# Performance work log

Measured on AMD Instinct MI355X. Metric: run time of the kernel, lower is better.

Reference implementation:

```python
import jax, jax.numpy as jnp
import numpy as np

LN_EPS = 1e-5  # torch nn.LayerNorm default
ATT_EPS = 1e-8  # episilon added to sqrt(dk)

B, S, D = 16, 2048, 1024


def setup_inputs() -> dict:
    key = jax.random.key(0)
    ks = jax.random.split(key, 5)
    Q = jax.random.normal(ks[0], (B, S, D), dtype=jnp.float32)
    K = jax.random.normal(ks[1], (B, S, D), dtype=jnp.float32)
    V = jax.random.normal(ks[2], (B, S, D), dtype=jnp.float32)
    # xavier_normal for square DxD: std = sqrt(2/(D+D)) = 1/sqrt(D)
    std = 1.0 / np.sqrt(D)
    W1 = jax.random.normal(ks[3], (D, D), dtype=jnp.float32) * std
    W2 = jax.random.normal(ks[4], (D, D), dtype=jnp.float32) * std
    b1 = jnp.zeros((D,), dtype=jnp.float32)
    b2 = jnp.zeros((D,), dtype=jnp.float32)
    ln_gamma = jnp.ones((D,), dtype=jnp.float32)
    ln_beta = jnp.zeros((D,), dtype=jnp.float32)
    return {"Q": Q, "K": K, "V": V, "W1": W1, "b1": b1, "W2": W2, "b2": b2,
            "ln_gamma": ln_gamma, "ln_beta": ln_beta}


def _layer_norm(x, gamma, beta):
    mu = jnp.mean(x, axis=-1, keepdims=True)
    var = jnp.mean(jnp.square(x - mu), axis=-1, keepdims=True)
    return (x - mu) * jax.lax.rsqrt(var + LN_EPS) * gamma + beta


def reference(Q, K, V, W1, b1, W2, b2, ln_gamma, ln_beta):
    d = Q.shape[-1]
    scale = 1.0 / (jnp.sqrt(jnp.float32(max(1.0, d))) + ATT_EPS)
    # scores: (B, Sq, Sk)
    scores = jnp.einsum('bqd,bkd->bqk', Q, K) * scale
    attn = jax.nn.softmax(scores, axis=-1)
    V_att = jnp.einsum('bqk,bkd->bqd', attn, V)
    X = _layer_norm(Q + V_att, ln_gamma, ln_beta)
    ffn = jnp.einsum('bqd,ed->bqe', jax.nn.relu(jnp.einsum('bqd,hd->bqh', X, W1) + b1), W2) + b2
    return _layer_norm(ffn + X, ln_gamma, ln_beta)
```

## Files before the change

### kernel.cpp

```cpp
#include <hip/hip_runtime.h>
#include <cmath>
#include <cstdint>

#define LN_EPS 1e-5f

typedef __bf16 bf16x8 __attribute__((ext_vector_type(8)));
typedef float f32x4 __attribute__((ext_vector_type(4)));
typedef unsigned short u16x8 __attribute__((ext_vector_type(8)));
typedef unsigned short u16x4 __attribute__((ext_vector_type(4)));

__device__ inline float b2f(unsigned short u) {
    union { unsigned int ui; float f; } x; x.ui = ((unsigned int)u) << 16; return x.f;
}
__device__ inline unsigned short f2b(float f) {
    union { float f; unsigned int ui; } x; x.f = f;
    unsigned int u = x.ui;
    return (unsigned short)((u + 0x7FFFu + ((u >> 16) & 1u)) >> 16);
}

__global__ void cvt_kernel(const float* __restrict__ in, unsigned short* __restrict__ out,
                           long n, float scale) {
    long i = ((long)blockIdx.x * blockDim.x + threadIdx.x) * 8;
    long stride = (long)gridDim.x * blockDim.x * 8;
    for (; i < n; i += stride) {
        float4 a = *reinterpret_cast<const float4*>(in + i);
        float4 b = *reinterpret_cast<const float4*>(in + i + 4);
        u16x8 o;
        o[0] = f2b(a.x * scale); o[1] = f2b(a.y * scale); o[2] = f2b(a.z * scale); o[3] = f2b(a.w * scale);
        o[4] = f2b(b.x * scale); o[5] = f2b(b.y * scale); o[6] = f2b(b.z * scale); o[7] = f2b(b.w * scale);
        *reinterpret_cast<u16x8*>(out + i) = o;
    }
}

__global__ void transpose_kernel(const float* __restrict__ V, unsigned short* __restrict__ Vt,
                                 int S, int D) {
    __shared__ float t[32][33];
    int b = blockIdx.z;
    int s0 = blockIdx.x * 32, d0 = blockIdx.y * 32;
    int tx = threadIdx.x & 31, ty = threadIdx.x >> 5;
    const float* Vb = V + (long)b * S * D;
    unsigned short* Vtb = Vt + (long)b * S * D;
#pragma unroll
    for (int r = 0; r < 4; ++r)
        t[ty + r * 8][tx] = Vb[(long)(s0 + ty + r * 8) * D + d0 + tx];
    __syncthreads();
#pragma unroll
    for (int r = 0; r < 4; ++r)
        Vtb[(long)(d0 + ty + r * 8) * S + s0 + tx] = f2b(t[tx][ty + r * 8]);
}

#define GBK 64

__device__ inline void gload16(const unsigned short* g, unsigned short* l) {
    __builtin_amdgcn_global_load_lds((const __attribute__((address_space(1))) void*)g,
                                     (__attribute__((address_space(3))) void*)l, 16, 0, 0);
}

__device__ inline void stage_half(const unsigned short* gRowBase, int ldk, int k0,
                                  unsigned short* ldsHalf, int tid) {
#pragma unroll
    for (int l = 0; l < 2; ++l) {
        int g = l * 512 + tid;
        int row = g >> 3;
        int lg = (g & 7) ^ (row & 7);
        gload16(gRowBase + (long)row * ldk + k0 + lg * 8, ldsHalf + g * 8);
    }
}

__device__ inline bf16x8 frag_ld(const unsigned short* ldsHalf, int rowInHalf, int kgran) {
    int sw = kgran ^ (rowInHalf & 7);
    return *reinterpret_cast<const bf16x8*>(ldsHalf + rowInHalf * 64 + sw * 8);
}

#define GMFMA(am, bn, mi, ni) \
    acc[mi][ni] = __builtin_amdgcn_mfma_f32_16x16x32_bf16(am, bn, acc[mi][ni], 0, 0, 0)

template <int MODE>
__global__ __launch_bounds__(512, 1) void gemm256(
    const unsigned short* __restrict__ A, const unsigned short* __restrict__ B,
    void* __restrict__ Cout, const float* __restrict__ aux1, const float* __restrict__ aux2,
    int N, int K, long bsA, long bsB, long bsC, float scale) {
    extern __shared__ __align__(16) unsigned short lds[];
    const int bz = blockIdx.z;
    const unsigned short* Ab = A + bz * bsA + (long)blockIdx.y * 256 * K;
    const unsigned short* Bb = B + bz * bsB + (long)blockIdx.x * 256 * K;
    const int tid = threadIdx.x;
    const int wid = tid >> 6, lane = tid & 63;
    const int wr = wid >> 2, wc = wid & 3;
    const int lr = lane & 15, kq = lane >> 4;
    const int NT = K / GBK;
    const int ccol = lane & 15, crow0 = kq * 4;
    const long m0 = (long)blockIdx.y * 256 + wr * 128;
    const long n0 = (long)blockIdx.x * 256 + wc * 64;

#define STAGE_A(tile, half) stage_half(Ab + (long)(half) * 128 * K, K, (tile) * GBK, \
        lds + (((tile) & 1) * 32768 + (half) * 8192), tid)
#define STAGE_B(tile, half) stage_half(Bb + (long)(half) * 128 * K, K, (tile) * GBK, \
        lds + (((tile) & 1) * 32768 + 16384 + (half) * 8192), tid)

    f32x4 acc[8][4];
#pragma unroll
    for (int i = 0; i < 8; ++i)
#pragma unroll
        for (int j = 0; j < 4; ++j) acc[i][j] = (f32x4){0.f, 0.f, 0.f, 0.f};
    bf16x8 a[4][2], b[4][2];

    STAGE_A(0, 0); STAGE_A(0, 1); STAGE_B(0, 0); STAGE_B(0, 1);
    STAGE_B(1, 0); STAGE_A(1, 0);
    asm volatile("s_waitcnt vmcnt(4)" ::: "memory");
    __builtin_amdgcn_s_barrier();

    for (int t = 0; t < NT; ++t) {
        const unsigned short* aB = lds + ((t & 1) * 32768 + wr * 8192);
        const unsigned short* bB = lds + ((t & 1) * 32768 + 16384 + (wc >> 1) * 8192);
        const int bRow0 = (wc & 1) * 64;
#pragma unroll
        for (int m = 0; m < 4; ++m)
#pragma unroll
            for (int ks = 0; ks < 2; ++ks)
                a[m][ks] = frag_ld(aB, m * 16 + lr, ks * 4 + kq);
#pragma unroll
        for (int n = 0; n < 2; ++n)
#pragma unroll
            for (int ks = 0; ks < 2; ++ks)
                b[n][ks] = frag_ld(bB, bRow0 + n * 16 + lr, ks * 4 + kq);
        if (t + 1 < NT) STAGE_A(t + 1, 1);
        __builtin_amdgcn_s_barrier();
        asm volatile("s_waitcnt lgkmcnt(0)" ::: "memory");
        __builtin_amdgcn_sched_barrier(0);
        __builtin_amdgcn_s_setprio(1);
#pragma unroll
        for (int m = 0; m < 4; ++m)
#pragma unroll
            for (int n = 0; n < 2; ++n)
#pragma unroll
                for (int ks = 0; ks < 2; ++ks) GMFMA(a[m][ks], b[n][ks], m, n);
        __builtin_amdgcn_s_setprio(0);
        __builtin_amdgcn_s_barrier();
#pragma unroll
        for (int n = 0; n < 2; ++n)
#pragma unroll
            for (int ks = 0; ks < 2; ++ks)
                b[2 + n][ks] = frag_ld(bB, bRow0 + (2 + n) * 16 + lr, ks * 4 + kq);
        if (t + 1 < NT) STAGE_B(t + 1, 1);
        __builtin_amdgcn_s_barrier();
        asm volatile("s_waitcnt lgkmcnt(0)" ::: "memory");
        __builtin_amdgcn_sched_barrier(0);
        __builtin_amdgcn_s_setprio(1);
#pragma unroll
        for (int m = 0; m < 4; ++m)
#pragma unroll
            for (int n = 0; n < 2; ++n)
#pragma unroll
                for (int ks = 0; ks < 2; ++ks) GMFMA(a[m][ks], b[2 + n][ks], m, 2 + n);
        __builtin_amdgcn_s_setprio(0);
        __builtin_amdgcn_s_barrier();
#pragma unroll
        for (int m = 0; m < 4; ++m)
#pragma unroll
            for (int ks = 0; ks < 2; ++ks)
                a[m][ks] = frag_ld(aB, 64 + m * 16 + lr, ks * 4 + kq);
        if (t + 2 < NT) STAGE_B(t + 2, 0);
        __builtin_amdgcn_s_barrier();
        asm volatile("s_waitcnt lgkmcnt(0)" ::: "memory");
        __builtin_amdgcn_sched_barrier(0);
        __builtin_amdgcn_s_setprio(1);
#pragma unroll
        for (int m = 0; m < 4; ++m)
#pragma unroll
            for (int n = 0; n < 2; ++n)
#pragma unroll
                for (int ks = 0; ks < 2; ++ks) GMFMA(a[m][ks], b[n][ks], 4 + m, n);
        __builtin_amdgcn_s_setprio(0);
        __builtin_amdgcn_s_barrier();
        if (t + 2 < NT) STAGE_A(t + 2, 0);
        if (t < NT - 2) asm volatile("s_waitcnt vmcnt(4)" ::: "memory");
        else            asm volatile("s_waitcnt vmcnt(0)" ::: "memory");
        __builtin_amdgcn_s_barrier();
        __builtin_amdgcn_s_setprio(1);
#pragma unroll
        for (int m = 0; m < 4; ++m)
#pragma unroll
            for (int n = 0; n < 2; ++n)
#pragma unroll
                for (int ks = 0; ks < 2; ++ks) GMFMA(a[m][ks], b[2 + n][ks], 4 + m, 2 + n);
        __builtin_amdgcn_s_setprio(0);
        __builtin_amdgcn_s_barrier();
    }

    if (MODE == 0) {
        float* sl = (float*)lds;
        unsigned short* Pout = (unsigned short*)Cout;
#pragma unroll
        for (int m = 0; m < 8; ++m) {
            float ls[4] = {0.f, 0.f, 0.f, 0.f};
#pragma unroll
            for (int n = 0; n < 4; ++n) {
                long gn = n0 + n * 16 + ccol;
#pragma unroll
                for (int r = 0; r < 4; ++r) {
                    float p = __expf(acc[m][n][r]);
                    ls[r] += p;
                    Pout[bz * bsC + (m0 + m * 16 + crow0 + r) * N + gn] = f2b(p);
                }
            }
#pragma unroll
            for (int r = 0; r < 4; ++r)
#pragma unroll
                for (int off = 8; off >= 1; off >>= 1) ls[r] += __shfl_xor(ls[r], off, 64);
            if ((lane & 15) == 0)
#pragma unroll
                for (int r = 0; r < 4; ++r)
                    sl[wc * 256 + wr * 128 + m * 16 + crow0 + r] = ls[r];
        }
        __syncthreads();
        if (wc == 0) {
#pragma unroll
            for (int rep = 0; rep < 2; ++rep) {
                int rowB = wr * 128 + rep * 64 + lane;
                float s4 = sl[0 * 256 + rowB] + sl[1 * 256 + rowB] +
                           sl[2 * 256 + rowB] + sl[3 * 256 + rowB];
                ((float*)aux1)[((long)bz * 8 + blockIdx.x) * 2048 + blockIdx.y * 256 + rowB] = s4;
            }
        }
        return;
    }

    if (MODE == 1) {
        const float* il = aux2 + (long)bz * 2048 + m0;
#pragma unroll
        for (int m = 0; m < 8; ++m)
#pragma unroll
            for (int r = 0; r < 4; ++r) {
                float cf = il[m * 16 + crow0 + r];
#pragma unroll
                for (int n = 0; n < 4; ++n) acc[m][n][r] *= cf;
            }
    }

#pragma unroll
    for (int m = 0; m < 8; ++m) {
#pragma unroll
        for (int n = 0; n < 4; ++n) {
            long gn = n0 + n * 16 + ccol;
#pragma unroll
            for (int r = 0; r < 4; ++r) {
                long gm = m0 + m * 16 + crow0 + r;
                float v = acc[m][n][r];
                if (MODE == 1) {
                    long idx = bz * bsC + gm * N + gn;
                    ((float*)Cout)[idx] = v + aux1[idx];
                } else if (MODE == 2) {
                    ((unsigned short*)Cout)[gm * N + gn] = f2b(fmaxf(v + aux1[gn], 0.f));
                } else {
                    long idx = gm * N + gn;
                    ((float*)Cout)[idx] = v + aux1[gn] + b2f(((const unsigned short*)aux2)[idx]);
                }
            }
        }
    }
#undef STAGE_A
#undef STAGE_B
}

__global__ void suminv_kernel(const float* __restrict__ stats, float* __restrict__ invL) {
    int i = blockIdx.x * 256 + threadIdx.x;
    int bz = i >> 11, row = i & 2047;
    long base = (long)bz * 8 * 2048 + row;
    float L = 0.f;
#pragma unroll
    for (int t = 0; t < 8; ++t) L += stats[base + t * 2048];
    invL[i] = 1.f / L;
}

__device__ inline float wave_sum(float v) {
#pragma unroll
    for (int off = 32; off > 0; off >>= 1) v += __shfl_xor(v, off, 64);
    return v;
}

template <bool WF32, bool WB16>
__global__ void ln_kernel(const float* __restrict__ X, const float* __restrict__ gamma,
                          const float* __restrict__ beta, float* __restrict__ outf,
                          unsigned short* __restrict__ outb) {
    __shared__ float red[8];
    long row = blockIdx.x;
    const float* x = X + row * 1024;
    int tid = threadIdx.x;
    int wv = tid >> 6, ln = tid & 63;
    float4 v = *reinterpret_cast<const float4*>(x + tid * 4);
    float s = v.x + v.y + v.z + v.w;
    float q = v.x * v.x + v.y * v.y + v.z * v.z + v.w * v.w;
    s = wave_sum(s);
    q = wave_sum(q);
    if (ln == 0) { red[wv] = s; red[4 + wv] = q; }
    __syncthreads();
    s = red[0] + red[1] + red[2] + red[3];
    q = red[4] + red[5] + red[6] + red[7];
    float mu = s * (1.f / 1024.f);
    float var = q * (1.f / 1024.f) - mu * mu;
    float rs = rsqrtf(var + LN_EPS);
    float4 g = *reinterpret_cast<const float4*>(gamma + tid * 4);
    float4 b = *reinterpret_cast<const float4*>(beta + tid * 4);
    float4 y;
    y.x = (v.x - mu) * rs * g.x + b.x;
    y.y = (v.y - mu) * rs * g.y + b.y;
    y.z = (v.z - mu) * rs * g.z + b.z;
    y.w = (v.w - mu) * rs * g.w + b.w;
    if (WF32)
        *reinterpret_cast<float4*>(outf + row * 1024 + tid * 4) = y;
    if (WB16) {
        u16x4 o;
        o[0] = f2b(y.x); o[1] = f2b(y.y); o[2] = f2b(y.z); o[3] = f2b(y.w);
        *reinterpret_cast<u16x4*>(outb + row * 1024 + tid * 4) = o;
    }
}

extern "C" void kernel_launch(void* const* d_in, const int* in_sizes, int n_in,
                              void* d_out, int out_size, void* d_ws, size_t ws_size,
                              hipStream_t stream) {
    const float* Q     = (const float*)d_in[0];
    const float* K     = (const float*)d_in[1];
    const float* V     = (const float*)d_in[2];
    const float* W1    = (const float*)d_in[3];
    const float* b1    = (const float*)d_in[4];
    const float* W2    = (const float*)d_in[5];
    const float* b2    = (const float*)d_in[6];
    const float* gamma = (const float*)d_in[7];
    const float* beta  = (const float*)d_in[8];
    float* out = (float*)d_out;

    const int Bq = 16, S = 2048, D = 1024;
    const long SD = (long)S * D;
    const long SS = (long)S * S;
    const long rows = (long)Bq * S;

    const size_t NEED = 3 * (size_t)(Bq * SD * 2) + 2 * (size_t)D * D * 2 + (size_t)(Bq * SS * 2);
    if (ws_size < NEED) return;

    char* ws = (char*)d_ws;
    unsigned short* Qb  = (unsigned short*)ws; ws += Bq * SD * 2;
    unsigned short* Kb  = (unsigned short*)ws; ws += Bq * SD * 2;
    unsigned short* Vt  = (unsigned short*)ws; ws += Bq * SD * 2;
    unsigned short* W1b = (unsigned short*)ws; ws += (long)D * D * 2;
    unsigned short* W2b = (unsigned short*)ws; ws += (long)D * D * 2;
    unsigned short* Sb  = (unsigned short*)ws; ws += Bq * SS * 2;

    unsigned short* Xb = Qb;
    unsigned short* H  = Kb;
    float*          Y  = (float*)Sb;
    float*          Xf = out;

    float* stats = (float*)W1b;
    float* invL  = stats + (long)Bq * 8 * 2048;

    (void)hipFuncSetAttribute(reinterpret_cast<const void*>(&gemm256<0>),
                              hipFuncAttributeMaxDynamicSharedMemorySize, 131072);
    (void)hipFuncSetAttribute(reinterpret_cast<const void*>(&gemm256<1>),
                              hipFuncAttributeMaxDynamicSharedMemorySize, 131072);
    (void)hipFuncSetAttribute(reinterpret_cast<const void*>(&gemm256<2>),
                              hipFuncAttributeMaxDynamicSharedMemorySize, 131072);
    (void)hipFuncSetAttribute(reinterpret_cast<const void*>(&gemm256<3>),
                              hipFuncAttributeMaxDynamicSharedMemorySize, 131072);

    const float scale = 1.0f / (sqrtf((float)D) + 1e-8f);

    cvt_kernel<<<1024, 256, 0, stream>>>(Q, Qb, Bq * SD, scale);
    cvt_kernel<<<1024, 256, 0, stream>>>(K, Kb, Bq * SD, 1.0f);
    transpose_kernel<<<dim3(S / 32, D / 32, Bq), 256, 0, stream>>>(V, Vt, S, D);

    gemm256<0><<<dim3(S / 256, S / 256, Bq), 512, 131072, stream>>>(
        Qb, Kb, Sb, stats, nullptr, S, D, SD, SD, SS, 1.0f);
    suminv_kernel<<<128, 256, 0, stream>>>(stats, invL);
    gemm256<1><<<dim3(D / 256, S / 256, Bq), 512, 131072, stream>>>(
        Sb, Vt, Xf, Q, invL, D, S, SS, SD, SD, 1.0f);

    ln_kernel<false, true><<<rows, 256, 0, stream>>>(Xf, gamma, beta, nullptr, Xb);

    cvt_kernel<<<512, 256, 0, stream>>>(W1, W1b, (long)D * D, 1.0f);
    cvt_kernel<<<512, 256, 0, stream>>>(W2, W2b, (long)D * D, 1.0f);

    gemm256<2><<<dim3(D / 256, rows / 256, 1), 512, 131072, stream>>>(
        Xb, W1b, H, b1, nullptr, D, D, 0, 0, 0, 1.0f);
    gemm256<3><<<dim3(D / 256, rows / 256, 1), 512, 131072, stream>>>(
        H, W2b, Y, b2, (const float*)Xb, D, D, 0, 0, 0, 1.0f);
    ln_kernel<true, false><<<rows, 256, 0, stream>>>(Y, gamma, beta, out, nullptr);
}
```

Baseline: 722.0 us.

## Make GEMM kernel persistent with cross-tile prefetch and restructured fragment pipeline

The GEMM kernel becomes persistent. Each block processes TPB consecutive output tiles on a 256-block grid, and the LDS double-buffer prefetch continues across tile boundaries so the next tile's loads overlap the current epilogue. The inner loop is reordered so the next k-step's A/B fragments are loaded before the last MFMA group, and the explicit lgkmcnt waits and sched barriers are removed. The attention-output epilogue now reads the residual from the scaled bf16 Q copy and rescales it, instead of reading fp32 Q, which adds some bf16 rounding error. The softmax stats scratch moves to an extra 4 KB of LDS so it does not clobber the staging buffers.

```diff
diff --git a/kernel.cpp b/kernel.cpp
--- a/kernel.cpp
+++ b/kernel.cpp
@@ -79,188 +79,235 @@
 __global__ __launch_bounds__(512, 1) void gemm256(
     const unsigned short* __restrict__ A, const unsigned short* __restrict__ B,
     void* __restrict__ Cout, const float* __restrict__ aux1, const float* __restrict__ aux2,
-    int N, int K, long bsA, long bsB, long bsC, float scale) {
+    int tX, int tY, int N, int K, long bsA, long bsB, long bsC, float scale, int TPB) {
     extern __shared__ __align__(16) unsigned short lds[];
-    const int bz = blockIdx.z;
-    const unsigned short* Ab = A + bz * bsA + (long)blockIdx.y * 256 * K;
-    const unsigned short* Bb = B + bz * bsB + (long)blockIdx.x * 256 * K;
     const int tid = threadIdx.x;
     const int wid = tid >> 6, lane = tid & 63;
     const int wr = wid >> 2, wc = wid & 3;
     const int lr = lane & 15, kq = lane >> 4;
-    const int NT = K / GBK;
+    const int NT = K >> 6;
+    const int totalKT = TPB * NT;
     const int ccol = lane & 15, crow0 = kq * 4;
-    const long m0 = (long)blockIdx.y * 256 + wr * 128;
-    const long n0 = (long)blockIdx.x * 256 + wc * 64;
-
-#define STAGE_A(tile, half) stage_half(Ab + (long)(half) * 128 * K, K, (tile) * GBK, \
-        lds + (((tile) & 1) * 32768 + (half) * 8192), tid)
-#define STAGE_B(tile, half) stage_half(Bb + (long)(half) * 128 * K, K, (tile) * GBK, \
-        lds + (((tile) & 1) * 32768 + 16384 + (half) * 8192), tid)
+    const int bRow0 = (wc & 1) * 64;
+
+    int tile = blockIdx.x * TPB;
+
+    auto tA = [&](int t) -> const unsigned short* {
+        int byz = t / tX; int by = byz % tY; int bz = byz / tY;
+        return A + (long)bz * bsA + (long)by * 256 * K;
+    };
+    auto tB = [&](int t) -> const unsigned short* {
+        int bx = t % tX; int byz = t / tX; int bz = byz / tY;
+        return B + (long)bz * bsB + (long)bx * 256 * K;
+    };
+    const unsigned short* AbC = tA(tile);
+    const unsigned short* BbC = tB(tile);
+    const unsigned short* AbN = (TPB > 1) ? tA(tile + 1) : AbC;
+    const unsigned short* BbN = (TPB > 1) ? tB(tile + 1) : BbC;
 
     f32x4 acc[8][4];
 #pragma unroll
     for (int i = 0; i < 8; ++i)
 #pragma unroll
         for (int j = 0; j < 4; ++j) acc[i][j] = (f32x4){0.f, 0.f, 0.f, 0.f};
-    bf16x8 a[4][2], b[4][2];
-
-    STAGE_A(0, 0); STAGE_A(0, 1); STAGE_B(0, 0); STAGE_B(0, 1);
-    STAGE_B(1, 0); STAGE_A(1, 0);
+    bf16x8 alo[4][2], ahi[4][2], b01[2][2], b23[2][2];
+
+    stage_half(AbC,                 K, 0,   lds,                 tid);
+    stage_half(AbC + (long)128 * K, K, 0,   lds + 8192,          tid);
+    stage_half(BbC,                 K, 0,   lds + 16384,         tid);
+    stage_half(BbC + (long)128 * K, K, 0,   lds + 24576,         tid);
+    stage_half(BbC,                 K, GBK, lds + 32768 + 16384, tid);
+    stage_half(AbC,                 K, GBK, lds + 32768,         tid);
     asm volatile("s_waitcnt vmcnt(4)" ::: "memory");
     __builtin_amdgcn_s_barrier();
 
-    for (int t = 0; t < NT; ++t) {
-        const unsigned short* aB = lds + ((t & 1) * 32768 + wr * 8192);
-        const unsigned short* bB = lds + ((t & 1) * 32768 + 16384 + (wc >> 1) * 8192);
-        const int bRow0 = (wc & 1) * 64;
-#pragma unroll
-        for (int m = 0; m < 4; ++m)
+    {
+        const unsigned short* aB = lds + wr * 8192;
+        const unsigned short* bB = lds + 16384 + (wc >> 1) * 8192;
+#pragma unroll
+        for (int m = 0; m < 4; ++m)
+#pragma unroll
+            for (int ks = 0; ks < 2; ++ks) alo[m][ks] = frag_ld(aB, m * 16 + lr, ks * 4 + kq);
+#pragma unroll
+        for (int n = 0; n < 2; ++n)
+#pragma unroll
+            for (int ks = 0; ks < 2; ++ks) b01[n][ks] = frag_ld(bB, bRow0 + n * 16 + lr, ks * 4 + kq);
+    }
+
+    int k = 0;
+    for (int gt = 0; gt < totalKT; ++gt, ++k) {
+        const unsigned short* aBc = lds + (gt & 1) * 32768 + wr * 8192;
+        const unsigned short* bBc = lds + (gt & 1) * 32768 + 16384 + (wc >> 1) * 8192;
+        unsigned short* buf1 = lds + ((gt + 1) & 1) * 32768;
+        unsigned short* buf2 = lds + (gt & 1) * 32768;
+        const bool s1 = (gt + 1 < totalKT), s2 = (gt + 2 < totalKT);
+        const bool in1 = (k + 1 < NT), in2 = (k + 2 < NT);
+        const unsigned short* A1 = in1 ? AbC : AbN;  const int kk1 = in1 ? k + 1 : 0;
+        const unsigned short* B1 = in1 ? BbC : BbN;
+        const unsigned short* A2 = in2 ? AbC : AbN;  const int kk2 = in2 ? k + 2 : k + 2 - NT;
+        const unsigned short* B2 = in2 ? BbC : BbN;
+
+        if (s1) stage_half(A1 + (long)128 * K, K, kk1 * GBK, buf1 + 8192, tid);
+#pragma unroll
+        for (int n = 0; n < 2; ++n)
 #pragma unroll
             for (int ks = 0; ks < 2; ++ks)
-                a[m][ks] = frag_ld(aB, m * 16 + lr, ks * 4 + kq);
-#pragma unroll
-        for (int n = 0; n < 2; ++n)
+                b23[n][ks] = frag_ld(bBc, bRow0 + (2 + n) * 16 + lr, ks * 4 + kq);
+        __builtin_amdgcn_s_barrier();
+        __builtin_amdgcn_s_setprio(1);
+#pragma unroll
+        for (int m = 0; m < 4; ++m)
+#pragma unroll
+            for (int n = 0; n < 2; ++n)
+#pragma unroll
+                for (int ks = 0; ks < 2; ++ks) GMFMA(alo[m][ks], b01[n][ks], m, n);
+        __builtin_amdgcn_s_setprio(0);
+        __builtin_amdgcn_s_barrier();
+
+        if (s1) stage_half(B1 + (long)128 * K, K, kk1 * GBK, buf1 + 24576, tid);
+#pragma unroll
+        for (int m = 0; m < 4; ++m)
 #pragma unroll
             for (int ks = 0; ks < 2; ++ks)
-                b[n][ks] = frag_ld(bB, bRow0 + n * 16 + lr, ks * 4 + kq);
-        if (t + 1 < NT) STAGE_A(t + 1, 1);
-        __builtin_amdgcn_s_barrier();
-        asm volatile("s_waitcnt lgkmcnt(0)" ::: "memory");
-        __builtin_amdgcn_sched_barrier(0);
+                ahi[m][ks] = frag_ld(aBc, 64 + m * 16 + lr, ks * 4 + kq);
+        __builtin_amdgcn_s_barrier();
         __builtin_amdgcn_s_setprio(1);
 #pragma unroll
         for (int m = 0; m < 4; ++m)
 #pragma unroll
             for (int n = 0; n < 2; ++n)
 #pragma unroll
-                for (int ks = 0; ks < 2; ++ks) GMFMA(a[m][ks], b[n][ks], m, n);
+                for (int ks = 0; ks < 2; ++ks) GMFMA(alo[m][ks], b23[n][ks], m, 2 + n);
         __builtin_amdgcn_s_setprio(0);
         __builtin_amdgcn_s_barrier();
-#pragma unroll
-        for (int n = 0; n < 2; ++n)
-#pragma unroll
-            for (int ks = 0; ks < 2; ++ks)
-                b[2 + n][ks] = frag_ld(bB, bRow0 + (2 + n) * 16 + lr, ks * 4 + kq);
-        if (t + 1 < NT) STAGE_B(t + 1, 1);
-        __builtin_amdgcn_s_barrier();
-        asm volatile("s_waitcnt lgkmcnt(0)" ::: "memory");
-        __builtin_amdgcn_sched_barrier(0);
+
+        if (s2) stage_half(B2, K, kk2 * GBK, buf2 + 16384, tid);
+        __builtin_amdgcn_s_barrier();
         __builtin_amdgcn_s_setprio(1);
 #pragma unroll
         for (int m = 0; m < 4; ++m)
 #pragma unroll
             for (int n = 0; n < 2; ++n)
 #pragma unroll
-                for (int ks = 0; ks < 2; ++ks) GMFMA(a[m][ks], b[2 + n][ks], m, 2 + n);
+                for (int ks = 0; ks < 2; ++ks) GMFMA(ahi[m][ks], b01[n][ks], 4 + m, n);
         __builtin_amdgcn_s_setprio(0);
         __builtin_amdgcn_s_barrier();
-#pragma unroll
-        for (int m = 0; m < 4; ++m)
-#pragma unroll
-            for (int ks = 0; ks < 2; ++ks)
-                a[m][ks] = frag_ld(aB, 64 + m * 16 + lr, ks * 4 + kq);
-        if (t + 2 < NT) STAGE_B(t + 2, 0);
-        __builtin_amdgcn_s_barrier();
-        asm volatile("s_waitcnt lgkmcnt(0)" ::: "memory");
-        __builtin_amdgcn_sched_barrier(0);
+
+        if (s2) stage_half(A2, K, kk2 * GBK, buf2, tid);
+        if (gt < totalKT - 2) asm volatile("s_waitcnt vmcnt(4)" ::: "memory");
+        else                  asm volatile("s_waitcnt vmcnt(0)" ::: "memory");
+        __builtin_amdgcn_s_barrier();
+        if (s1) {
+            const unsigned short* aBn = buf1 + wr * 8192;
+            const unsigned short* bBn = buf1 + 16384 + (wc >> 1) * 8192;
+#pragma unroll
+            for (int m = 0; m < 4; ++m)
+#pragma unroll
+                for (int ks = 0; ks < 2; ++ks) alo[m][ks] = frag_ld(aBn, m * 16 + lr, ks * 4 + kq);
+#pragma unroll
+            for (int n = 0; n < 2; ++n)
+#pragma unroll
+                for (int ks = 0; ks < 2; ++ks) b01[n][ks] = frag_ld(bBn, bRow0 + n * 16 + lr, ks * 4 + kq);
+        }
         __builtin_amdgcn_s_setprio(1);
 #pragma unroll
         for (int m = 0; m < 4; ++m)
 #pragma unroll
             for (int n = 0; n < 2; ++n)
 #pragma unroll
-                for (int ks = 0; ks < 2; ++ks) GMFMA(a[m][ks], b[n][ks], 4 + m, n);
+                for (int ks = 0; ks < 2; ++ks) GMFMA(ahi[m][ks], b23[n][ks], 4 + m, 2 + n);
         __builtin_amdgcn_s_setprio(0);
         __builtin_amdgcn_s_barrier();
-        if (t + 2 < NT) STAGE_A(t + 2, 0);
-        if (t < NT - 2) asm volatile("s_waitcnt vmcnt(4)" ::: "memory");
-        else            asm volatile("s_waitcnt vmcnt(0)" ::: "memory");
-        __builtin_amdgcn_s_barrier();
-        __builtin_amdgcn_s_setprio(1);
-#pragma unroll
-        for (int m = 0; m < 4; ++m)
-#pragma unroll
-            for (int n = 0; n < 2; ++n)
-#pragma unroll
-                for (int ks = 0; ks < 2; ++ks) GMFMA(a[m][ks], b[2 + n][ks], 4 + m, 2 + n);
-        __builtin_amdgcn_s_setprio(0);
-        __builtin_amdgcn_s_barrier();
-    }
-
-    if (MODE == 0) {
-        float* sl = (float*)lds;
-        unsigned short* Pout = (unsigned short*)Cout;
-#pragma unroll
-        for (int m = 0; m < 8; ++m) {
-            float ls[4] = {0.f, 0.f, 0.f, 0.f};
-#pragma unroll
-            for (int n = 0; n < 4; ++n) {
-                long gn = n0 + n * 16 + ccol;
-#pragma unroll
-                for (int r = 0; r < 4; ++r) {
-                    float p = __expf(acc[m][n][r]);
-                    ls[r] += p;
-                    Pout[bz * bsC + (m0 + m * 16 + crow0 + r) * N + gn] = f2b(p);
+
+        if (k == NT - 1) {
+            const int bx = tile % tX;
+            const int byz = tile / tX;
+            const int by = byz % tY;
+            const int bz = byz / tY;
+            const long m0 = (long)by * 256 + wr * 128;
+            const long n0 = (long)bx * 256 + wc * 64;
+
+            if (MODE == 0) {
+                float* sl = (float*)(lds + 65536);
+                unsigned short* Pout = (unsigned short*)Cout;
+#pragma unroll
+                for (int m = 0; m < 8; ++m) {
+                    float ls[4] = {0.f, 0.f, 0.f, 0.f};
+#pragma unroll
+                    for (int n = 0; n < 4; ++n) {
+                        long gn = n0 + n * 16 + ccol;
+#pragma unroll
+                        for (int r = 0; r < 4; ++r) {
+                            float p = __expf(acc[m][n][r]);
+                            ls[r] += p;
+                            Pout[bz * bsC + (m0 + m * 16 + crow0 + r) * N + gn] = f2b(p);
+                        }
+                    }
+#pragma unroll
+                    for (int r = 0; r < 4; ++r)
+#pragma unroll
+                        for (int off = 8; off >= 1; off >>= 1) ls[r] += __shfl_xor(ls[r], off, 64);
+                    if ((lane & 15) == 0)
+#pragma unroll
+                        for (int r = 0; r < 4; ++r)
+                            sl[wc * 256 + wr * 128 + m * 16 + crow0 + r] = ls[r];
+                }
+                __syncthreads();
+                if (wc == 0) {
+#pragma unroll
+                    for (int rep = 0; rep < 2; ++rep) {
+                        int rowB = wr * 128 + rep * 64 + lane;
+                        float s4 = sl[0 * 256 + rowB] + sl[1 * 256 + rowB] +
+                                   sl[2 * 256 + rowB] + sl[3 * 256 + rowB];
+                        ((float*)aux1)[((long)bz * 8 + bx) * 2048 + by * 256 + rowB] = s4;
+                    }
+                }
+            } else {
+                if (MODE == 1) {
+                    const float* il = aux2 + (long)bz * 2048 + m0;
+#pragma unroll
+                    for (int m = 0; m < 8; ++m)
+#pragma unroll
+                        for (int r = 0; r < 4; ++r) {
+                            float cf = il[m * 16 + crow0 + r];
+#pragma unroll
+                            for (int n = 0; n < 4; ++n) acc[m][n][r] *= cf;
+                        }
+                }
+#pragma unroll
+                for (int m = 0; m < 8; ++m) {
+#pragma unroll
+                    for (int n = 0; n < 4; ++n) {
+                        long gn = n0 + n * 16 + ccol;
+#pragma unroll
+                        for (int r = 0; r < 4; ++r) {
+                            long gm = m0 + m * 16 + crow0 + r;
+                            float v = acc[m][n][r];
+                            if (MODE == 1) {
+                                long idx = bz * bsC + gm * N + gn;
+                                ((float*)Cout)[idx] =
+                                    v + b2f(((const unsigned short*)aux1)[idx]) * scale;
+                            } else if (MODE == 2) {
+                                ((unsigned short*)Cout)[gm * N + gn] = f2b(fmaxf(v + aux1[gn], 0.f));
+                            } else {
+                                long idx = gm * N + gn;
+                                ((float*)Cout)[idx] =
+                                    v + aux1[gn] + b2f(((const unsigned short*)aux2)[idx]);
+                            }
+                        }
+                    }
                 }
             }
 #pragma unroll
-            for (int r = 0; r < 4; ++r)
-#pragma unroll
-                for (int off = 8; off >= 1; off >>= 1) ls[r] += __shfl_xor(ls[r], off, 64);
-            if ((lane & 15) == 0)
-#pragma unroll
-                for (int r = 0; r < 4; ++r)
-                    sl[wc * 256 + wr * 128 + m * 16 + crow0 + r] = ls[r];
-        }
-        __syncthreads();
-        if (wc == 0) {
-#pragma unroll
-            for (int rep = 0; rep < 2; ++rep) {
-                int rowB = wr * 128 + rep * 64 + lane;
-                float s4 = sl[0 * 256 + rowB] + sl[1 * 256 + rowB] +
-                           sl[2 * 256 + rowB] + sl[3 * 256 + rowB];
-                ((float*)aux1)[((long)bz * 8 + blockIdx.x) * 2048 + blockIdx.y * 256 + rowB] = s4;
-            }
-        }
-        return;
-    }
-
-    if (MODE == 1) {
-        const float* il = aux2 + (long)bz * 2048 + m0;
-#pragma unroll
-        for (int m = 0; m < 8; ++m)
-#pragma unroll
-            for (int r = 0; r < 4; ++r) {
-                float cf = il[m * 16 + crow0 + r];
-#pragma unroll
-                for (int n = 0; n < 4; ++n) acc[m][n][r] *= cf;
-            }
-    }
-
-#pragma unroll
-    for (int m = 0; m < 8; ++m) {
-#pragma unroll
-        for (int n = 0; n < 4; ++n) {
-            long gn = n0 + n * 16 + ccol;
-#pragma unroll
-            for (int r = 0; r < 4; ++r) {
-                long gm = m0 + m * 16 + crow0 + r;
-                float v = acc[m][n][r];
-                if (MODE == 1) {
-                    long idx = bz * bsC + gm * N + gn;
-                    ((float*)Cout)[idx] = v + aux1[idx];
-                } else if (MODE == 2) {
-                    ((unsigned short*)Cout)[gm * N + gn] = f2b(fmaxf(v + aux1[gn], 0.f));
-                } else {
-                    long idx = gm * N + gn;
-                    ((float*)Cout)[idx] = v + aux1[gn] + b2f(((const unsigned short*)aux2)[idx]);
-                }
-            }
+            for (int i = 0; i < 8; ++i)
+#pragma unroll
+                for (int j = 0; j < 4; ++j) acc[i][j] = (f32x4){0.f, 0.f, 0.f, 0.f};
+            ++tile;
+            AbC = AbN; BbC = BbN;
+            if (tile + 1 < (blockIdx.x + 1) * TPB) { AbN = tA(tile + 1); BbN = tB(tile + 1); }
+            k = -1;
         }
     }
-#undef STAGE_A
-#undef STAGE_B
 }
 
 __global__ void suminv_kernel(const float* __restrict__ stats, float* __restrict__ invL) {
@@ -354,35 +401,37 @@
     float* stats = (float*)W1b;
     float* invL  = stats + (long)Bq * 8 * 2048;
 
+    const int DYN_LDS = 131072 + 4096;
     (void)hipFuncSetAttribute(reinterpret_cast<const void*>(&gemm256<0>),
-                              hipFuncAttributeMaxDynamicSharedMemorySize, 131072);
+                              hipFuncAttributeMaxDynamicSharedMemorySize, DYN_LDS);
     (void)hipFuncSetAttribute(reinterpret_cast<const void*>(&gemm256<1>),
-                              hipFuncAttributeMaxDynamicSharedMemorySize, 131072);
+                              hipFuncAttributeMaxDynamicSharedMemorySize, DYN_LDS);
     (void)hipFuncSetAttribute(reinterpret_cast<const void*>(&gemm256<2>),
-                              hipFuncAttributeMaxDynamicSharedMemorySize, 131072);
+                              hipFuncAttributeMaxDynamicSharedMemorySize, DYN_LDS);
     (void)hipFuncSetAttribute(reinterpret_cast<const void*>(&gemm256<3>),
-                              hipFuncAttributeMaxDynamicSharedMemorySize, 131072);
+                              hipFuncAttributeMaxDynamicSharedMemorySize, DYN_LDS);
 
     const float scale = 1.0f / (sqrtf((float)D) + 1e-8f);
+    const float rescale = sqrtf((float)D) + 1e-8f;
 
     cvt_kernel<<<1024, 256, 0, stream>>>(Q, Qb, Bq * SD, scale);
     cvt_kernel<<<1024, 256, 0, stream>>>(K, Kb, Bq * SD, 1.0f);
     transpose_kernel<<<dim3(S / 32, D / 32, Bq), 256, 0, stream>>>(V, Vt, S, D);
 
-    gemm256<0><<<dim3(S / 256, S / 256, Bq), 512, 131072, stream>>>(
-        Qb, Kb, Sb, stats, nullptr, S, D, SD, SD, SS, 1.0f);
+    gemm256<0><<<256, 512, DYN_LDS, stream>>>(
+        Qb, Kb, Sb, stats, nullptr, 8, 8, S, D, SD, SD, SS, 1.0f, 4);
     suminv_kernel<<<128, 256, 0, stream>>>(stats, invL);
-    gemm256<1><<<dim3(D / 256, S / 256, Bq), 512, 131072, stream>>>(
-        Sb, Vt, Xf, Q, invL, D, S, SS, SD, SD, 1.0f);
+    gemm256<1><<<256, 512, DYN_LDS, stream>>>(
+        Sb, Vt, Xf, (const float*)Qb, invL, 4, 8, D, S, SS, SD, SD, rescale, 2);
 
     ln_kernel<false, true><<<rows, 256, 0, stream>>>(Xf, gamma, beta, nullptr, Xb);
 
     cvt_kernel<<<512, 256, 0, stream>>>(W1, W1b, (long)D * D, 1.0f);
     cvt_kernel<<<512, 256, 0, stream>>>(W2, W2b, (long)D * D, 1.0f);
 
-    gemm256<2><<<dim3(D / 256, rows / 256, 1), 512, 131072, stream>>>(
-        Xb, W1b, H, b1, nullptr, D, D, 0, 0, 0, 1.0f);
-    gemm256<3><<<dim3(D / 256, rows / 256, 1), 512, 131072, stream>>>(
-        H, W2b, Y, b2, (const float*)Xb, D, D, 0, 0, 0, 1.0f);
+    gemm256<2><<<256, 512, DYN_LDS, stream>>>(
+        Xb, W1b, H, b1, nullptr, 4, 128, D, D, 0, 0, 0, 1.0f, 2);
+    gemm256<3><<<256, 512, DYN_LDS, stream>>>(
+        H, W2b, Y, b2, (const float*)Xb, 4, 128, D, D, 0, 0, 0, 1.0f, 2);
     ln_kernel<true, false><<<rows, 256, 0, stream>>>(Y, gamma, beta, out, nullptr);
 }
```

Measured after the change: 728.4 us. Within noise of the previous version (+0.9%).

## Fuse LayerNorm statistics into PV GEMM epilogue, use bf16 intermediates and XCD block swizzle

Applied to the files above, without the earlier changes.

The PV GEMM epilogue now adds the residual, read back from the scaled bf16 Q and rescaled, and writes bf16 X directly. It also computes per-row partial sums and sums of squares, so the separate fp32 LayerNorm pass over X becomes a small stats reduction plus an in-place bf16 apply. The final FFN GEMM writes a bf16 Y instead of fp32, which halves that traffic. All GEMMs move to a 1D grid with a block-index swizzle that groups blocks across the eight XCDs for L2 locality. The residual Q now passes through a bf16 round-trip with scaling, and Y is stored in bf16, which adds some precision error.

```diff
diff --git a/kernel.cpp b/kernel.cpp
--- a/kernel.cpp
+++ b/kernel.cpp
@@ -79,19 +79,26 @@
 __global__ __launch_bounds__(512, 1) void gemm256(
     const unsigned short* __restrict__ A, const unsigned short* __restrict__ B,
     void* __restrict__ Cout, const float* __restrict__ aux1, const float* __restrict__ aux2,
-    int N, int K, long bsA, long bsB, long bsC, float scale) {
+    float* __restrict__ aux3, float* __restrict__ aux4,
+    int tX, int tY, int N, int K, long bsA, long bsB, long bsC, float scale) {
     extern __shared__ __align__(16) unsigned short lds[];
-    const int bz = blockIdx.z;
-    const unsigned short* Ab = A + bz * bsA + (long)blockIdx.y * 256 * K;
-    const unsigned short* Bb = B + bz * bsB + (long)blockIdx.x * 256 * K;
+    const int cpx = gridDim.x >> 3;
+    const int swz = (blockIdx.x & 7) * cpx + (blockIdx.x >> 3);
+    const int bx = swz % tX;
+    const int t2 = swz / tX;
+    const int by = t2 % tY;
+    const int bz = t2 / tY;
+
+    const unsigned short* Ab = A + (long)bz * bsA + (long)by * 256 * K;
+    const unsigned short* Bb = B + (long)bz * bsB + (long)bx * 256 * K;
     const int tid = threadIdx.x;
     const int wid = tid >> 6, lane = tid & 63;
     const int wr = wid >> 2, wc = wid & 3;
     const int lr = lane & 15, kq = lane >> 4;
-    const int NT = K / GBK;
+    const int NT = K >> 6;
     const int ccol = lane & 15, crow0 = kq * 4;
-    const long m0 = (long)blockIdx.y * 256 + wr * 128;
-    const long n0 = (long)blockIdx.x * 256 + wc * 64;
+    const long m0 = (long)by * 256 + wr * 128;
+    const long n0 = (long)bx * 256 + wc * 64;
 
 #define STAGE_A(tile, half) stage_half(Ab + (long)(half) * 128 * K, K, (tile) * GBK, \
         lds + (((tile) & 1) * 32768 + (half) * 8192), tid)
@@ -220,7 +227,7 @@
                 int rowB = wr * 128 + rep * 64 + lane;
                 float s4 = sl[0 * 256 + rowB] + sl[1 * 256 + rowB] +
                            sl[2 * 256 + rowB] + sl[3 * 256 + rowB];
-                ((float*)aux1)[((long)bz * 8 + blockIdx.x) * 2048 + blockIdx.y * 256 + rowB] = s4;
+                ((float*)aux1)[((long)bz * 8 + bx) * 2048 + by * 256 + rowB] = s4;
             }
         }
         return;
@@ -228,14 +235,53 @@
 
     if (MODE == 1) {
         const float* il = aux2 + (long)bz * 2048 + m0;
-#pragma unroll
-        for (int m = 0; m < 8; ++m)
+        float* sls = (float*)lds;
+        float* slq = sls + 1024;
+        unsigned short* Xout = (unsigned short*)Cout;
+#pragma unroll
+        for (int m = 0; m < 8; ++m) {
+            float ls[4] = {0.f, 0.f, 0.f, 0.f}, lq[4] = {0.f, 0.f, 0.f, 0.f};
 #pragma unroll
             for (int r = 0; r < 4; ++r) {
                 float cf = il[m * 16 + crow0 + r];
-#pragma unroll
-                for (int n = 0; n < 4; ++n) acc[m][n][r] *= cf;
+                long gm = m0 + m * 16 + crow0 + r;
+#pragma unroll
+                for (int n = 0; n < 4; ++n) {
+                    long gn = n0 + n * 16 + ccol;
+                    long idx = bz * bsC + gm * N + gn;
+                    float v = acc[m][n][r] * cf +
+                              b2f(((const unsigned short*)aux1)[idx]) * scale;
+                    Xout[idx] = f2b(v);
+                    ls[r] += v; lq[r] += v * v;
+                }
             }
+#pragma unroll
+            for (int r = 0; r < 4; ++r)
+#pragma unroll
+                for (int off = 8; off >= 1; off >>= 1) {
+                    ls[r] += __shfl_xor(ls[r], off, 64);
+                    lq[r] += __shfl_xor(lq[r], off, 64);
+                }
+            if ((lane & 15) == 0)
+#pragma unroll
+                for (int r = 0; r < 4; ++r) {
+                    sls[wc * 256 + wr * 128 + m * 16 + crow0 + r] = ls[r];
+                    slq[wc * 256 + wr * 128 + m * 16 + crow0 + r] = lq[r];
+                }
+        }
+        __syncthreads();
+        if (wc == 0) {
+#pragma unroll
+            for (int rep = 0; rep < 2; ++rep) {
+                int rowB = wr * 128 + rep * 64 + lane;
+                float s4 = sls[rowB] + sls[256 + rowB] + sls[512 + rowB] + sls[768 + rowB];
+                float q4 = slq[rowB] + slq[256 + rowB] + slq[512 + rowB] + slq[768 + rowB];
+                long sidx = ((long)bz * 4 + bx) * 2048 + by * 256 + rowB;
+                aux3[sidx] = s4;
+                aux4[sidx] = q4;
+            }
+        }
+        return;
     }
 
 #pragma unroll
@@ -247,14 +293,12 @@
             for (int r = 0; r < 4; ++r) {
                 long gm = m0 + m * 16 + crow0 + r;
                 float v = acc[m][n][r];
-                if (MODE == 1) {
-                    long idx = bz * bsC + gm * N + gn;
-                    ((float*)Cout)[idx] = v + aux1[idx];
-                } else if (MODE == 2) {
+                if (MODE == 2) {
                     ((unsigned short*)Cout)[gm * N + gn] = f2b(fmaxf(v + aux1[gn], 0.f));
                 } else {
                     long idx = gm * N + gn;
-                    ((float*)Cout)[idx] = v + aux1[gn] + b2f(((const unsigned short*)aux2)[idx]);
+                    ((unsigned short*)Cout)[idx] =
+                        f2b(v + aux1[gn] + b2f(((const unsigned short*)aux2)[idx]));
                 }
             }
         }
@@ -273,24 +317,61 @@
     invL[i] = 1.f / L;
 }
 
+__global__ void lnstats_kernel(const float* __restrict__ ss, const float* __restrict__ sq,
+                               float* __restrict__ mu, float* __restrict__ rs) {
+    int i = blockIdx.x * 256 + threadIdx.x;
+    int bz = i >> 11, row = i & 2047;
+    long base = (long)bz * 4 * 2048 + row;
+    float s = 0.f, q = 0.f;
+#pragma unroll
+    for (int t = 0; t < 4; ++t) { s += ss[base + t * 2048]; q += sq[base + t * 2048]; }
+    float m = s * (1.f / 1024.f);
+    float var = q * (1.f / 1024.f) - m * m;
+    mu[i] = m;
+    rs[i] = rsqrtf(var + LN_EPS);
+}
+
+__global__ void ln_apply_kernel(unsigned short* __restrict__ X, const float* __restrict__ mu,
+                                const float* __restrict__ rs, const float* __restrict__ gamma,
+                                const float* __restrict__ beta) {
+    long i = ((long)blockIdx.x * 256 + threadIdx.x) * 8;
+    int row = (int)(i >> 10), col = (int)(i & 1023);
+    float m = mu[row], r = rs[row];
+    u16x8 raw = *reinterpret_cast<const u16x8*>(X + i);
+    float4 g0 = *reinterpret_cast<const float4*>(gamma + col);
+    float4 g1 = *reinterpret_cast<const float4*>(gamma + col + 4);
+    float4 b0 = *reinterpret_cast<const float4*>(beta + col);
+    float4 b1 = *reinterpret_cast<const float4*>(beta + col + 4);
+    u16x8 o;
+    o[0] = f2b((b2f(raw[0]) - m) * r * g0.x + b0.x);
+    o[1] = f2b((b2f(raw[1]) - m) * r * g0.y + b0.y);
+    o[2] = f2b((b2f(raw[2]) - m) * r * g0.z + b0.z);
+    o[3] = f2b((b2f(raw[3]) - m) * r * g0.w + b0.w);
+    o[4] = f2b((b2f(raw[4]) - m) * r * g1.x + b1.x);
+    o[5] = f2b((b2f(raw[5]) - m) * r * g1.y + b1.y);
+    o[6] = f2b((b2f(raw[6]) - m) * r * g1.z + b1.z);
+    o[7] = f2b((b2f(raw[7]) - m) * r * g1.w + b1.w);
+    *reinterpret_cast<u16x8*>(X + i) = o;
+}
+
 __device__ inline float wave_sum(float v) {
 #pragma unroll
     for (int off = 32; off > 0; off >>= 1) v += __shfl_xor(v, off, 64);
     return v;
 }
 
-template <bool WF32, bool WB16>
-__global__ void ln_kernel(const float* __restrict__ X, const float* __restrict__ gamma,
-                          const float* __restrict__ beta, float* __restrict__ outf,
-                          unsigned short* __restrict__ outb) {
+__global__ void ln_final_kernel(const unsigned short* __restrict__ Yb,
+                                const float* __restrict__ gamma, const float* __restrict__ beta,
+                                float* __restrict__ out) {
     __shared__ float red[8];
     long row = blockIdx.x;
-    const float* x = X + row * 1024;
+    const unsigned short* y = Yb + row * 1024;
     int tid = threadIdx.x;
     int wv = tid >> 6, ln = tid & 63;
-    float4 v = *reinterpret_cast<const float4*>(x + tid * 4);
-    float s = v.x + v.y + v.z + v.w;
-    float q = v.x * v.x + v.y * v.y + v.z * v.z + v.w * v.w;
+    u16x4 raw = *reinterpret_cast<const u16x4*>(y + tid * 4);
+    float v0 = b2f(raw[0]), v1 = b2f(raw[1]), v2 = b2f(raw[2]), v3 = b2f(raw[3]);
+    float s = v0 + v1 + v2 + v3;
+    float q = v0 * v0 + v1 * v1 + v2 * v2 + v3 * v3;
     s = wave_sum(s);
     q = wave_sum(q);
     if (ln == 0) { red[wv] = s; red[4 + wv] = q; }
@@ -299,21 +380,15 @@
     q = red[4] + red[5] + red[6] + red[7];
     float mu = s * (1.f / 1024.f);
     float var = q * (1.f / 1024.f) - mu * mu;
-    float rs = rsqrtf(var + LN_EPS);
+    float rsg = rsqrtf(var + LN_EPS);
     float4 g = *reinterpret_cast<const float4*>(gamma + tid * 4);
     float4 b = *reinterpret_cast<const float4*>(beta + tid * 4);
-    float4 y;
-    y.x = (v.x - mu) * rs * g.x + b.x;
-    y.y = (v.y - mu) * rs * g.y + b.y;
-    y.z = (v.z - mu) * rs * g.z + b.z;
-    y.w = (v.w - mu) * rs * g.w + b.w;
-    if (WF32)
-        *reinterpret_cast<float4*>(outf + row * 1024 + tid * 4) = y;
-    if (WB16) {
-        u16x4 o;
-        o[0] = f2b(y.x); o[1] = f2b(y.y); o[2] = f2b(y.z); o[3] = f2b(y.w);
-        *reinterpret_cast<u16x4*>(outb + row * 1024 + tid * 4) = o;
-    }
+    float4 o;
+    o.x = (v0 - mu) * rsg * g.x + b.x;
+    o.y = (v1 - mu) * rsg * g.y + b.y;
+    o.z = (v2 - mu) * rsg * g.z + b.z;
+    o.w = (v3 - mu) * rsg * g.w + b.w;
+    *reinterpret_cast<float4*>(out + row * 1024 + tid * 4) = o;
 }
 
 extern "C" void kernel_launch(void* const* d_in, const int* in_sizes, int n_in,
@@ -348,41 +423,48 @@
 
     unsigned short* Xb = Qb;
     unsigned short* H  = Kb;
-    float*          Y  = (float*)Sb;
-    float*          Xf = out;
-
-    float* stats = (float*)W1b;
-    float* invL  = stats + (long)Bq * 8 * 2048;
-
+    unsigned short* Yb = (unsigned short*)Sb;
+
+    char* sc = (char*)W1b;
+    float* stats   = (float*)sc;
+    float* invL    = (float*)(sc + 0x100000);
+    float* stats_s = (float*)(sc + 0x140000);
+    float* stats_q = (float*)(sc + 0x1C0000);
+    float* muArr   = (float*)(sc + 0x240000);
+    float* rsArr   = (float*)(sc + 0x260000);
+
+    const int DYN_LDS = 131072;
     (void)hipFuncSetAttribute(reinterpret_cast<const void*>(&gemm256<0>),
-                              hipFuncAttributeMaxDynamicSharedMemorySize, 131072);
+                              hipFuncAttributeMaxDynamicSharedMemorySize, DYN_LDS);
     (void)hipFuncSetAttribute(reinterpret_cast<const void*>(&gemm256<1>),
-                              hipFuncAttributeMaxDynamicSharedMemorySize, 131072);
+                              hipFuncAttributeMaxDynamicSharedMemorySize, DYN_LDS);
     (void)hipFuncSetAttribute(reinterpret_cast<const void*>(&gemm256<2>),
-                              hipFuncAttributeMaxDynamicSharedMemorySize, 131072);
+                              hipFuncAttributeMaxDynamicSharedMemorySize, DYN_LDS);
     (void)hipFuncSetAttribute(reinterpret_cast<const void*>(&gemm256<3>),
-                              hipFuncAttributeMaxDynamicSharedMemorySize, 131072);
+                              hipFuncAttributeMaxDynamicSharedMemorySize, DYN_LDS);
 
     const float scale = 1.0f / (sqrtf((float)D) + 1e-8f);
+    const float rescale = sqrtf((float)D) + 1e-8f;
 
     cvt_kernel<<<1024, 256, 0, stream>>>(Q, Qb, Bq * SD, scale);
     cvt_kernel<<<1024, 256, 0, stream>>>(K, Kb, Bq * SD, 1.0f);
     transpose_kernel<<<dim3(S / 32, D / 32, Bq), 256, 0, stream>>>(V, Vt, S, D);
 
-    gemm256<0><<<dim3(S / 256, S / 256, Bq), 512, 131072, stream>>>(
-        Qb, Kb, Sb, stats, nullptr, S, D, SD, SD, SS, 1.0f);
+    gemm256<0><<<1024, 512, DYN_LDS, stream>>>(
+        Qb, Kb, Sb, stats, nullptr, nullptr, nullptr, 8, 8, S, D, SD, SD, SS, 1.0f);
     suminv_kernel<<<128, 256, 0, stream>>>(stats, invL);
-    gemm256<1><<<dim3(D / 256, S / 256, Bq), 512, 131072, stream>>>(
-        Sb, Vt, Xf, Q, invL, D, S, SS, SD, SD, 1.0f);
-
-    ln_kernel<false, true><<<rows, 256, 0, stream>>>(Xf, gamma, beta, nullptr, Xb);
+
+    gemm256<1><<<512, 512, DYN_LDS, stream>>>(
+        Sb, Vt, Xb, (const float*)Qb, invL, stats_s, stats_q, 4, 8, D, S, SS, SD, SD, rescale);
+    lnstats_kernel<<<128, 256, 0, stream>>>(stats_s, stats_q, muArr, rsArr);
+    ln_apply_kernel<<<16384, 256, 0, stream>>>(Xb, muArr, rsArr, gamma, beta);
 
     cvt_kernel<<<512, 256, 0, stream>>>(W1, W1b, (long)D * D, 1.0f);
     cvt_kernel<<<512, 256, 0, stream>>>(W2, W2b, (long)D * D, 1.0f);
 
-    gemm256<2><<<dim3(D / 256, rows / 256, 1), 512, 131072, stream>>>(
-        Xb, W1b, H, b1, nullptr, D, D, 0, 0, 0, 1.0f);
-    gemm256<3><<<dim3(D / 256, rows / 256, 1), 512, 131072, stream>>>(
-        H, W2b, Y, b2, (const float*)Xb, D, D, 0, 0, 0, 1.0f);
-    ln_kernel<true, false><<<rows, 256, 0, stream>>>(Y, gamma, beta, out, nullptr);
-}
+    gemm256<2><<<512, 512, DYN_LDS, stream>>>(
+        Xb, W1b, H, b1, nullptr, nullptr, nullptr, 4, 128, D, D, 0, 0, 0, 1.0f);
+    gemm256<3><<<512, 512, DYN_LDS, stream>>>(
+        H, W2b, Yb, b2, (const float*)Xb, nullptr, nullptr, 4, 128, D, D, 0, 0, 0, 1.0f);
+    ln_final_kernel<<<rows, 256, 0, stream>>>(Yb, gamma, beta, out);
+}
```

Measured after the change: 629.4 us. 12.8% less time.
